# Optimization experiments

Measured on AMD Instinct MI355X. Metric: run time of the kernel, lower is better.

The kernel has to match this reference:

```python
import jax, jax.numpy as jnp
import numpy as np

HIDDEN = 2048
NHEADS = 16
NKV = 4
HEAD_DIM = 128
B, T = 2, 2048


def setup_inputs() -> dict:
    key = jax.random.key(0)
    ks = jax.random.split(key, 7)
    x = jax.random.normal(ks[0], (B, T, HIDDEN), dtype=jnp.float32)
    # rope tables [T, head_dim//2]
    inv_freq = 1.0 / (10000.0 ** (jnp.arange(0, HEAD_DIM // 2, dtype=jnp.float32) / (HEAD_DIM // 2)))
    pos = jnp.arange(T, dtype=jnp.float32)
    ang = pos[:, None] * inv_freq[None, :]
    cos, sin = jnp.cos(ang), jnp.sin(ang)
    s = 0.02
    wq = jax.random.normal(ks[1], (HIDDEN, NHEADS * HEAD_DIM), dtype=jnp.float32) * s
    wk = jax.random.normal(ks[2], (HIDDEN, NKV * HEAD_DIM), dtype=jnp.float32) * s
    wv = jax.random.normal(ks[3], (HIDDEN, NKV * HEAD_DIM), dtype=jnp.float32) * s
    wo = jax.random.normal(ks[4], (NHEADS * HEAD_DIM, HIDDEN), dtype=jnp.float32) * s
    return {"x": x, "cos": cos, "sin": sin, "wq": wq, "wk": wk, "wv": wv, "wo": wo}


def _apply_rope(x, cos, sin):
    # x: [B, H, T, D]; cos/sin: [T, D//2]
    hd = x.shape[-1]
    x1, x2 = x[..., : hd // 2], x[..., hd // 2 :]
    c = cos[None, None, : x.shape[2], :]
    s = sin[None, None, : x.shape[2], :]
    return jnp.concatenate([x1 * c - x2 * s, x2 * c + x1 * s], axis=-1)


def reference(x, cos, sin, wq, wk, wv, wo):
    Bb, Tt, _ = x.shape
    q = (x @ wq).reshape(Bb, Tt, NHEADS, HEAD_DIM).transpose(0, 2, 1, 3)  # [B,H,T,D]
    k = (x @ wk).reshape(Bb, Tt, NKV, HEAD_DIM).transpose(0, 2, 1, 3)    # [B,Hk,T,D]
    v = (x @ wv).reshape(Bb, Tt, NKV, HEAD_DIM).transpose(0, 2, 1, 3)
    q = _apply_rope(q, cos, sin)
    k = _apply_rope(k, cos, sin)
    groups = NHEADS // NKV
    k = jnp.repeat(k, groups, axis=1)  # [B,H,T,D]
    v = jnp.repeat(v, groups, axis=1)
    scale = 1.0 / jnp.sqrt(jnp.asarray(HEAD_DIM, dtype=x.dtype))
    scores = jnp.einsum("bhqd,bhkd->bhqk", q, k) * scale
    causal = jnp.tril(jnp.ones((Tt, Tt), dtype=bool))
    scores = jnp.where(causal[None, None, :, :], scores, jnp.asarray(-jnp.inf, dtype=scores.dtype))
    attn = jax.nn.softmax(scores, axis=-1)
    out = jnp.einsum("bhqk,bhkd->bhqd", attn, v)
    out = out.transpose(0, 2, 1, 3).reshape(Bb, Tt, NHEADS * HEAD_DIM)
    return out @ wo
```

## Files before the change

kernel.cpp:

```cpp
#include <hip/hip_runtime.h>

#define HIDDEN 2048
#define NHEADS 16
#define NKV 4
#define HEAD_DIM 128
#define BB 2
#define TT 2048
#define MROWS (BB * TT)
#define NQKV (NHEADS * HEAD_DIM + 2 * NKV * HEAD_DIM)

typedef __attribute__((ext_vector_type(8))) short short8;
typedef __attribute__((ext_vector_type(4))) float f32x4;

#if __has_builtin(__builtin_amdgcn_exp2f)
#define EXP2F __builtin_amdgcn_exp2f
#else
#define EXP2F exp2f
#endif

__device__ __forceinline__ unsigned short f2bf(float f) {
    unsigned int u = __float_as_uint(f);
    unsigned int r = u + 0x7fffu + ((u >> 16) & 1u);
    return (unsigned short)(r >> 16);
}
__device__ __forceinline__ float b2f(unsigned short h) {
    return __uint_as_float(((unsigned int)h) << 16);
}

__device__ __forceinline__ void load_lds_16(const void* g, void* l) {
    __builtin_amdgcn_global_load_lds((const __attribute__((address_space(1))) unsigned int*)g,
                                     (__attribute__((address_space(3))) unsigned int*)l,
                                     16, 0, 0);
}

__global__ void cast_x_kernel(const float* __restrict__ x, unsigned short* __restrict__ xb) {
    int i = blockIdx.x * 256 + threadIdx.x;
    float4 v = ((const float4*)x)[i];
    ushort4 o;
    o.x = f2bf(v.x); o.y = f2bf(v.y); o.z = f2bf(v.z); o.w = f2bf(v.w);
    ((ushort4*)xb)[i] = o;
}

__global__ void pack_wqkvT_kernel(const float* __restrict__ wq, const float* __restrict__ wk,
                                  const float* __restrict__ wv, unsigned short* __restrict__ out) {
    __shared__ float tile[32][33];
    int n0 = blockIdx.x * 32, k0 = blockIdx.y * 32;
    int tx = threadIdx.x, ty = threadIdx.y;
#pragma unroll
    for (int i = 0; i < 32; i += 8) {
        int k = k0 + ty + i;
        int n = n0 + tx;
        float v;
        if (n < 2048)      v = wq[(size_t)k * 2048 + n];
        else if (n < 2560) v = wk[(size_t)k * 512 + (n - 2048)];
        else               v = wv[(size_t)k * 512 + (n - 2560)];
        tile[ty + i][tx] = v;
    }
    __syncthreads();
#pragma unroll
    for (int i = 0; i < 32; i += 8) {
        int n = n0 + ty + i;
        int k = k0 + tx;
        out[(size_t)n * HIDDEN + k] = f2bf(tile[tx][ty + i]);
    }
}

__global__ void pack_woT_kernel(const float* __restrict__ wo, unsigned short* __restrict__ out) {
    __shared__ float tile[32][33];
    int n0 = blockIdx.x * 32, k0 = blockIdx.y * 32;
    int tx = threadIdx.x, ty = threadIdx.y;
#pragma unroll
    for (int i = 0; i < 32; i += 8)
        tile[ty + i][tx] = wo[(size_t)(k0 + ty + i) * HIDDEN + n0 + tx];
    __syncthreads();
#pragma unroll
    for (int i = 0; i < 32; i += 8)
        out[(size_t)(n0 + ty + i) * HIDDEN + k0 + tx] = f2bf(tile[tx][ty + i]);
}

__global__ __launch_bounds__(512, 2) void gemm192_kernel(const unsigned short* __restrict__ A,
                                                         const unsigned short* __restrict__ Bt,
                                                         unsigned short* __restrict__ C) {
    const int N = NQKV, K = HIDDEN, NBX = 16;
    __shared__ __align__(16) unsigned short sA[2][256 * 64];
    __shared__ __align__(16) unsigned short sB[2][192 * 64];
    const int tid = threadIdx.x;
    const int lane = tid & 63, w = tid >> 6;
    const int quad = lane >> 4, l15 = lane & 15;
    const int wrM = w >> 2, wcN = w & 3;

    const int nwg = gridDim.x;
    const int bswz = (blockIdx.x & 7) * (nwg >> 3) + (blockIdx.x >> 3);
    const int m0 = (bswz / NBX) * 256;
    const int n0 = (bswz % NBX) * 192;

    const int lr = tid >> 3;
    const int sc = (tid & 7) ^ (lr & 7);
    const unsigned short* gA = A + (size_t)(m0 + lr) * K + sc * 8;
    const unsigned short* gB = Bt + (size_t)(n0 + lr) * K + sc * 8;
    const size_t jstep = (size_t)64 * K;

    const int s0 = (quad ^ (l15 & 7)) * 8;
    const int s1 = ((4 | quad) ^ (l15 & 7)) * 8;

    f32x4 acc[8][3];
    const f32x4 z4 = {0.f, 0.f, 0.f, 0.f};
#pragma unroll
    for (int mi = 0; mi < 8; ++mi)
#pragma unroll
        for (int ni = 0; ni < 3; ++ni) acc[mi][ni] = z4;

#pragma unroll
    for (int j = 0; j < 4; ++j)
        load_lds_16(gA + (size_t)j * jstep, &sA[0][j * 4096 + w * 512]);
#pragma unroll
    for (int j = 0; j < 3; ++j)
        load_lds_16(gB + (size_t)j * jstep, &sB[0][j * 4096 + w * 512]);

    const int NT = K >> 6;
    for (int kt = 0; kt < NT; ++kt) {
        const int buf = kt & 1;
        const unsigned short* bA = &sA[buf][0];
        const unsigned short* bB = &sB[buf][0];

        __builtin_amdgcn_s_barrier();
        if (kt + 1 < NT) {
            const size_t kof = (size_t)(kt + 1) * 64;
#pragma unroll
            for (int j = 0; j < 4; ++j)
                load_lds_16(gA + (size_t)j * jstep + kof, &sA[buf ^ 1][j * 4096 + w * 512]);
#pragma unroll
            for (int j = 0; j < 3; ++j)
                load_lds_16(gB + (size_t)j * jstep + kof, &sB[buf ^ 1][j * 4096 + w * 512]);
            __asm__ volatile("s_waitcnt vmcnt(7)" ::: "memory");
        } else {
            __asm__ volatile("s_waitcnt vmcnt(0)" ::: "memory");
        }
        __builtin_amdgcn_s_barrier();

        short8 bf0[3], bf1[3];
#pragma unroll
        for (int ni = 0; ni < 3; ++ni) {
            const unsigned short* br = bB + (wcN * 48 + ni * 16 + l15) * 64;
            bf0[ni] = *(const short8*)(br + s0);
            bf1[ni] = *(const short8*)(br + s1);
        }
#pragma unroll
        for (int ph = 0; ph < 4; ++ph) {
            short8 af0[2], af1[2];
#pragma unroll
            for (int mm = 0; mm < 2; ++mm) {
                const unsigned short* ar = bA + (wrM * 128 + (ph * 2 + mm) * 16 + l15) * 64;
                af0[mm] = *(const short8*)(ar + s0);
                af1[mm] = *(const short8*)(ar + s1);
            }
#pragma unroll
            for (int mm = 0; mm < 2; ++mm)
#pragma unroll
                for (int ni = 0; ni < 3; ++ni) {
                    acc[ph * 2 + mm][ni] =
                        __builtin_amdgcn_mfma_f32_16x16x32_bf16(af0[mm], bf0[ni], acc[ph * 2 + mm][ni], 0, 0, 0);
                    acc[ph * 2 + mm][ni] =
                        __builtin_amdgcn_mfma_f32_16x16x32_bf16(af1[mm], bf1[ni], acc[ph * 2 + mm][ni], 0, 0, 0);
                }
        }
    }

#pragma unroll
    for (int mi = 0; mi < 8; ++mi)
#pragma unroll
        for (int ni = 0; ni < 3; ++ni)
#pragma unroll
            for (int r = 0; r < 4; ++r) {
                int gr = m0 + wrM * 128 + mi * 16 + quad * 4 + r;
                int gc = n0 + wcN * 48 + ni * 16 + l15;
                C[(size_t)gr * N + gc] = f2bf(acc[mi][ni][r]);
            }
}

__global__ __launch_bounds__(512, 2) void gemm256n128_kernel(const unsigned short* __restrict__ A,
                                                             const unsigned short* __restrict__ Bt,
                                                             float* __restrict__ C,
                                                             int M, int N, int K, int NBX) {
    __shared__ __align__(16) unsigned short sA[2][256 * 64];
    __shared__ __align__(16) unsigned short sB[2][128 * 64];
    const int tid = threadIdx.x;
    const int lane = tid & 63, w = tid >> 6;
    const int quad = lane >> 4, l15 = lane & 15;
    const int wrM = w >> 1, wcN = w & 1;

    const int nwg = gridDim.x;
    const int bswz = (blockIdx.x & 7) * (nwg >> 3) + (blockIdx.x >> 3);
    const int m0 = (bswz / NBX) * 256;
    const int n0 = (bswz % NBX) * 128;

    const int lr = tid >> 3;
    const int sc = (tid & 7) ^ (lr & 7);
    const unsigned short* gA = A + (size_t)(m0 + lr) * K + sc * 8;
    const unsigned short* gB = Bt + (size_t)(n0 + lr) * K + sc * 8;
    const size_t jstep = (size_t)64 * K;

    const int s0 = (quad ^ (l15 & 7)) * 8;
    const int s1 = ((4 | quad) ^ (l15 & 7)) * 8;

    f32x4 acc[4][4];
    const f32x4 z4 = {0.f, 0.f, 0.f, 0.f};
#pragma unroll
    for (int mi = 0; mi < 4; ++mi)
#pragma unroll
        for (int ni = 0; ni < 4; ++ni) acc[mi][ni] = z4;

#pragma unroll
    for (int j = 0; j < 4; ++j)
        load_lds_16(gA + (size_t)j * jstep, &sA[0][j * 4096 + w * 512]);
#pragma unroll
    for (int j = 0; j < 2; ++j)
        load_lds_16(gB + (size_t)j * jstep, &sB[0][j * 4096 + w * 512]);

    const int NT = K >> 6;
    for (int kt = 0; kt < NT; ++kt) {
        const int buf = kt & 1;
        const unsigned short* bA = &sA[buf][0];
        const unsigned short* bB = &sB[buf][0];

        __builtin_amdgcn_s_barrier();
        if (kt + 1 < NT) {
            const size_t kof = (size_t)(kt + 1) * 64;
#pragma unroll
            for (int j = 0; j < 4; ++j)
                load_lds_16(gA + (size_t)j * jstep + kof, &sA[buf ^ 1][j * 4096 + w * 512]);
#pragma unroll
            for (int j = 0; j < 2; ++j)
                load_lds_16(gB + (size_t)j * jstep + kof, &sB[buf ^ 1][j * 4096 + w * 512]);
            __asm__ volatile("s_waitcnt vmcnt(6)" ::: "memory");
        } else {
            __asm__ volatile("s_waitcnt vmcnt(0)" ::: "memory");
        }
        __builtin_amdgcn_s_barrier();

        short8 bf0[4], bf1[4];
#pragma unroll
        for (int ni = 0; ni < 4; ++ni) {
            const unsigned short* br = bB + (wcN * 64 + ni * 16 + l15) * 64;
            bf0[ni] = *(const short8*)(br + s0);
            bf1[ni] = *(const short8*)(br + s1);
        }
#pragma unroll
        for (int ph = 0; ph < 4; ++ph) {
            short8 af0, af1;
            {
                const unsigned short* ar = bA + (wrM * 64 + ph * 16 + l15) * 64;
                af0 = *(const short8*)(ar + s0);
                af1 = *(const short8*)(ar + s1);
            }
#pragma unroll
            for (int ni = 0; ni < 4; ++ni) {
                acc[ph][ni] = __builtin_amdgcn_mfma_f32_16x16x32_bf16(af0, bf0[ni], acc[ph][ni], 0, 0, 0);
                acc[ph][ni] = __builtin_amdgcn_mfma_f32_16x16x32_bf16(af1, bf1[ni], acc[ph][ni], 0, 0, 0);
            }
        }
    }

#pragma unroll
    for (int mi = 0; mi < 4; ++mi)
#pragma unroll
        for (int ni = 0; ni < 4; ++ni)
#pragma unroll
            for (int r = 0; r < 4; ++r) {
                int gr = m0 + wrM * 64 + mi * 16 + quad * 4 + r;
                int gc = n0 + wcN * 64 + ni * 16 + l15;
                C[(size_t)gr * N + gc] = acc[mi][ni][r];
            }
}

#define QP (MROWS * NHEADS * 64)
#define KP (MROWS * NKV * 64)
#define QSCL (0.08838834764831845f * 1.4426950408889634f)
__global__ void rope_kernel(const unsigned short* __restrict__ qkv,
                            const float* __restrict__ cosb, const float* __restrict__ sinb,
                            unsigned short* __restrict__ Q, unsigned short* __restrict__ K) {
    int tid = blockIdx.x * 256 + threadIdx.x;
    if (tid < QP) {
        int d = tid & 63;
        int h = (tid >> 6) & 15;
        int row = tid >> 10;
        int t = row & (TT - 1), b = row >> 11;
        float x1 = b2f(qkv[(size_t)row * NQKV + h * 128 + d]);
        float x2 = b2f(qkv[(size_t)row * NQKV + h * 128 + d + 64]);
        float c = cosb[t * 64 + d], s = sinb[t * 64 + d];
        unsigned short* dst = Q + ((size_t)(b * NHEADS + h) * TT + t) * 128 + d;
        dst[0]  = f2bf((x1 * c - x2 * s) * QSCL);
        dst[64] = f2bf((x2 * c + x1 * s) * QSCL);
    } else {
        int p = tid - QP;
        int d = p & 63;
        int kh = (p >> 6) & 3;
        int row = p >> 8;
        int t = row & (TT - 1), b = row >> 11;
        float x1 = b2f(qkv[(size_t)row * NQKV + 2048 + kh * 128 + d]);
        float x2 = b2f(qkv[(size_t)row * NQKV + 2048 + kh * 128 + d + 64]);
        float c = cosb[t * 64 + d], s = sinb[t * 64 + d];
        unsigned short* dst = K + ((size_t)(b * NKV + kh) * TT + t) * 128 + d;
        dst[0]  = f2bf(x1 * c - x2 * s);
        dst[64] = f2bf(x2 * c + x1 * s);
    }
}

__global__ void vtrans_kernel(const unsigned short* __restrict__ qkv,
                              unsigned short* __restrict__ Vt) {
    __shared__ unsigned short tile[32][33];
    int t0 = blockIdx.x * 32, d0 = blockIdx.y * 32, bz = blockIdx.z;
    int b = bz >> 2, kh = bz & 3;
    int tx = threadIdx.x, ty = threadIdx.y;
#pragma unroll
    for (int i = 0; i < 32; i += 8)
        tile[ty + i][tx] = qkv[(size_t)(b * TT + t0 + ty + i) * NQKV + 2560 + kh * 128 + d0 + tx];
    __syncthreads();
#pragma unroll
    for (int i = 0; i < 32; i += 8)
        Vt[((size_t)bz * 128 + d0 + ty + i) * TT + t0 + tx] = tile[tx][ty + i];
}

__global__ __launch_bounds__(256, 3) void flash_kernel(const unsigned short* __restrict__ Qb,
                                                       const unsigned short* __restrict__ Kb,
                                                       const unsigned short* __restrict__ Vtb,
                                                       unsigned short* __restrict__ Ob,
                                                       unsigned short* __restrict__ Po,
                                                       float* __restrict__ Pl) {
    __shared__ __align__(16) unsigned short sK[2][64 * 128];
    __shared__ __align__(16) unsigned short sV[128 * 64];

    const int tid = threadIdx.x;
    const int w = tid >> 6, lane = tid & 63;
    const int quad = lane >> 4, l15 = lane & 15;
    const int r7 = l15 & 7;

    const int lin = blockIdx.x;
    const int member = lin >> 8;
    const int rem = lin & 255;
    const int h = rem & 15;
    const int b = (rem >> 4) & 1;
    const int j = rem >> 5;
    int qb, kvlo, kvhi;
    bool partial;
    if (member == 2) {
        qb = j; kvlo = 0; kvhi = (qb + 1) * 128; partial = false;
    } else {
        qb = 15 - j;
        int half = (qb + 1) * 64;
        kvlo = member ? half : 0;
        kvhi = member ? (qb + 1) * 128 : half;
        partial = true;
    }
    const int q0 = qb * 128;
    const int ntile = (kvhi - kvlo) >> 6;
    const int kvh = h >> 2;
    const unsigned short* Qh = Qb + (size_t)(b * NHEADS + h) * TT * 128;
    const unsigned short* Kh = Kb + (size_t)(b * NKV + kvh) * TT * 128;
    const unsigned short* Vth = Vtb + (size_t)(b * NKV + kvh) * 128 * TT;

    const int wrow0 = q0 + w * 32;

    const int kr = lane >> 4;
    const unsigned short* gKe = Kh + (size_t)(w * 16 + kr) * 128 + (((lane & 15) ^ kr) * 8);
    const unsigned short* gKo = Kh + (size_t)(w * 16 + 4 + kr) * 128 + (((lane & 15) ^ (4 + kr)) * 8);
    const int vr = lane >> 3;
    const unsigned short* gV0 = Vth + (size_t)(w * 32 + vr) * TT + (((lane & 7) ^ vr) * 8);

    short8 aq[2][4];
#pragma unroll
    for (int mi = 0; mi < 2; ++mi)
#pragma unroll
        for (int dk = 0; dk < 4; ++dk)
            aq[mi][dk] = *(const short8*)(Qh + (size_t)(wrow0 + mi * 16 + l15) * 128 + dk * 32 + quad * 8);

    f32x4 accO[2][8];
    float accLc[2] = {0.f, 0.f};
    const f32x4 z4 = {0.f, 0.f, 0.f, 0.f};
#pragma unroll
    for (int mi = 0; mi < 2; ++mi)
#pragma unroll
        for (int nb = 0; nb < 8; ++nb) accO[mi][nb] = z4;

#pragma unroll
    for (int g = 0; g < 4; ++g) {
        const unsigned short* src = (g & 1) ? gKo : gKe;
        load_lds_16(src + (size_t)(kvlo + (g >> 1) * 8) * 128, &sK[0][(w * 4 + g) * 512]);
    }

    for (int it = 0; it < ntile; ++it) {
        const int cur = it & 1;
        const int kv0 = kvlo + it * 64;
        __asm__ volatile("s_waitcnt vmcnt(0)" ::: "memory");
        __builtin_amdgcn_s_barrier();
#pragma unroll
        for (int g = 0; g < 4; ++g)
            load_lds_16(gV0 + (size_t)(g * 8) * TT + kv0, &sV[(w * 4 + g) * 512]);
        const bool hasn = (it + 1 < ntile);
        if (hasn) {
#pragma unroll
            for (int g = 0; g < 4; ++g) {
                const unsigned short* src = (g & 1) ? gKo : gKe;
                load_lds_16(src + (size_t)(kv0 + 64 + (g >> 1) * 8) * 128, &sK[cur ^ 1][(w * 4 + g) * 512]);
            }
        }
        const bool compute = (kv0 <= wrow0 + 31);
        short8 ap[2][2];
        if (compute) {
            f32x4 st[4][2];
#pragma unroll
            for (int t = 0; t < 4; ++t)
#pragma unroll
                for (int h2 = 0; h2 < 2; ++h2) st[t][h2] = z4;
            __builtin_amdgcn_s_setprio(1);
#pragma unroll
            for (int t = 0; t < 4; ++t) {
#pragma unroll
                for (int dk = 0; dk < 4; ++dk) {
                    short8 ak = *(const short8*)(&sK[cur][(t * 16 + l15) * 128 + ((dk * 4 + quad) ^ r7) * 8]);
                    st[t][0] = __builtin_amdgcn_mfma_f32_16x16x32_bf16(ak, aq[0][dk], st[t][0], 0, 0, 0);
                    st[t][1] = __builtin_amdgcn_mfma_f32_16x16x32_bf16(ak, aq[1][dk], st[t][1], 0, 0, 0);
                }
            }
            __builtin_amdgcn_s_setprio(0);
            unsigned int pk32[4][2][2];
#pragma unroll
            for (int h2 = 0; h2 < 2; ++h2) {
                const int qg = wrow0 + h2 * 16 + l15;
#pragma unroll
                for (int t = 0; t < 4; ++t) {
                    const int kvb = kv0 + t * 16 + quad * 4;
                    const bool nm = (kv0 + t * 16 + 15) > (wrow0 + h2 * 16);
                    float pv[4];
#pragma unroll
                    for (int r = 0; r < 4; ++r) {
                        float p = EXP2F(st[t][h2][r]);
                        if (nm) p = (kvb + r <= qg) ? p : 0.f;
                        pv[r] = p;
                    }
                    accLc[h2] += (pv[0] + pv[1]) + (pv[2] + pv[3]);
                    __asm__("v_cvt_pk_bf16_f32 %0, %1, %2" : "=v"(pk32[t][h2][0]) : "v"(pv[0]), "v"(pv[1]));
                    __asm__("v_cvt_pk_bf16_f32 %0, %1, %2" : "=v"(pk32[t][h2][1]) : "v"(pv[2]), "v"(pv[3]));
                }
            }
#pragma unroll
            for (int h2 = 0; h2 < 2; ++h2)
#pragma unroll
                for (int kf = 0; kf < 2; ++kf) {
                    union { unsigned int u[4]; short8 s8; } W;
#pragma unroll
                    for (int wdx = 0; wdx < 4; ++wdx) {
                        int srcl = (2 * (quad & 1) + (wdx >> 1)) * 16 + l15;
                        unsigned int a0 = (unsigned int)__shfl((int)pk32[2 * kf][h2][wdx & 1], srcl, 64);
                        unsigned int a1 = (unsigned int)__shfl((int)pk32[2 * kf + 1][h2][wdx & 1], srcl, 64);
                        W.u[wdx] = (quad >> 1) ? a1 : a0;
                    }
                    ap[h2][kf] = W.s8;
                }
        }
        if (hasn) { __asm__ volatile("s_waitcnt vmcnt(4)" ::: "memory"); }
        else      { __asm__ volatile("s_waitcnt vmcnt(0)" ::: "memory"); }
        __builtin_amdgcn_s_barrier();
        if (compute) {
            __builtin_amdgcn_s_setprio(1);
#pragma unroll
            for (int nb = 0; nb < 8; ++nb) {
                short8 bv0 = *(const short8*)(&sV[(nb * 16 + l15) * 64 + ((quad) ^ r7) * 8]);
                short8 bv1 = *(const short8*)(&sV[(nb * 16 + l15) * 64 + ((4 + quad) ^ r7) * 8]);
#pragma unroll
                for (int mi = 0; mi < 2; ++mi) {
                    accO[mi][nb] = __builtin_amdgcn_mfma_f32_16x16x32_bf16(ap[mi][0], bv0, accO[mi][nb], 0, 0, 0);
                    accO[mi][nb] = __builtin_amdgcn_mfma_f32_16x16x32_bf16(ap[mi][1], bv1, accO[mi][nb], 0, 0, 0);
                }
            }
            __builtin_amdgcn_s_setprio(0);
        }
    }

    float Lr[2][4];
#pragma unroll
    for (int mi = 0; mi < 2; ++mi) {
        float v = accLc[mi];
        v += __shfl_xor(v, 16, 64);
        v += __shfl_xor(v, 32, 64);
#pragma unroll
        for (int r = 0; r < 4; ++r)
            Lr[mi][r] = __shfl(v, quad * 4 + r, 64);
    }

    __syncthreads();
    unsigned short* sPw = &sV[0] + w * 2048;

    if (!partial) {
        float inv[2][4];
#pragma unroll
        for (int mi = 0; mi < 2; ++mi)
#pragma unroll
            for (int r = 0; r < 4; ++r) inv[mi][r] = 1.0f / Lr[mi][r];
        const size_t obase = ((size_t)b * TT + wrow0) * (NHEADS * HEAD_DIM) + h * 128;
#pragma unroll
        for (int half = 0; half < 2; ++half) {
            __asm__ volatile("s_waitcnt lgkmcnt(0)" ::: "memory");
#pragma unroll
            for (int mi = 0; mi < 2; ++mi)
#pragma unroll
                for (int nb2 = 0; nb2 < 4; ++nb2)
#pragma unroll
                    for (int r = 0; r < 4; ++r) {
                        const int row = mi * 16 + quad * 4 + r;
                        sPw[row * 64 + (((2 * nb2 + (l15 >> 3)) ^ (row & 7)) * 8) + r7] =
                            f2bf(accO[mi][half * 4 + nb2][r] * inv[mi][r]);
                    }
            __asm__ volatile("s_waitcnt lgkmcnt(0)" ::: "memory");
#pragma unroll
            for (int pass = 0; pass < 4; ++pass) {
                int row2 = pass * 8 + (lane >> 3);
                short8 vv = *(const short8*)(&sPw[row2 * 64 + (((lane & 7) ^ (row2 & 7)) * 8)]);
                *(short8*)(Ob + obase + (size_t)row2 * (NHEADS * HEAD_DIM) + half * 64 + (lane & 7) * 8) = vv;
            }
        }
    } else {
        const size_t pbase = ((size_t)(member * 2 + b) * 1024 + (wrow0 - 1024)) * 2048 + h * 128;
#pragma unroll
        for (int half = 0; half < 2; ++half) {
            __asm__ volatile("s_waitcnt lgkmcnt(0)" ::: "memory");
#pragma unroll
            for (int mi = 0; mi < 2; ++mi)
#pragma unroll
                for (int nb2 = 0; nb2 < 4; ++nb2)
#pragma unroll
                    for (int r = 0; r < 4; ++r) {
                        const int row = mi * 16 + quad * 4 + r;
                        sPw[row * 64 + (((2 * nb2 + (l15 >> 3)) ^ (row & 7)) * 8) + r7] =
                            f2bf(accO[mi][half * 4 + nb2][r]);
                    }
            __asm__ volatile("s_waitcnt lgkmcnt(0)" ::: "memory");
#pragma unroll
            for (int pass = 0; pass < 4; ++pass) {
                int row2 = pass * 8 + (lane >> 3);
                short8 vv = *(const short8*)(&sPw[row2 * 64 + (((lane & 7) ^ (row2 & 7)) * 8)]);
                *(short8*)(Po + pbase + (size_t)row2 * 2048 + half * 64 + (lane & 7) * 8) = vv;
            }
        }
        float* plb = Pl + ((size_t)(member * 2 + b) * 16 + h) * 1024 + (wrow0 - 1024);
        if (l15 == 0) {
#pragma unroll
            for (int mi = 0; mi < 2; ++mi)
#pragma unroll
                for (int r = 0; r < 4; ++r)
                    plb[mi * 16 + quad * 4 + r] = Lr[mi][r];
        }
    }
}

__global__ void merge_kernel(const unsigned short* __restrict__ Po, const float* __restrict__ Pl,
                             unsigned short* __restrict__ attn) {
    int gid = blockIdx.x * 256 + threadIdx.x;
    size_t e8 = (size_t)gid * 8;
    int col = (int)(e8 & 2047);
    int rl  = (int)((e8 >> 11) & 1023);
    int b   = (int)(e8 >> 21);
    int h   = col >> 7;
    size_t i0 = ((size_t)b * 1024 + rl) * 2048 + col;
    size_t i1 = ((size_t)(2 + b) * 1024 + rl) * 2048 + col;
    float l = Pl[((size_t)b * 16 + h) * 1024 + rl] + Pl[((size_t)(2 + b) * 16 + h) * 1024 + rl];
    float inv = 1.0f / l;
    union { uint4 v; unsigned short u[8]; } a, c, o;
    a.v = *(const uint4*)(Po + i0);
    c.v = *(const uint4*)(Po + i1);
#pragma unroll
    for (int k = 0; k < 8; ++k)
        o.u[k] = f2bf((b2f(a.u[k]) + b2f(c.u[k])) * inv);
    *(uint4*)(attn + ((size_t)b * 2048 + 1024 + rl) * 2048 + col) = o.v;
}

extern "C" void kernel_launch(void* const* d_in, const int* in_sizes, int n_in,
                              void* d_out, int out_size, void* d_ws, size_t ws_size,
                              hipStream_t stream) {
    const float* x    = (const float*)d_in[0];
    const float* cosb = (const float*)d_in[1];
    const float* sinb = (const float*)d_in[2];
    const float* wq   = (const float*)d_in[3];
    const float* wk   = (const float*)d_in[4];
    const float* wv   = (const float*)d_in[5];
    const float* wo   = (const float*)d_in[6];
    float* out = (float*)d_out;

    char* ws = (char*)d_ws;
    unsigned short* xb    = (unsigned short*)(ws);
    unsigned short* wqkvT = (unsigned short*)(ws + (16u << 20));
    unsigned short* woT   = (unsigned short*)(ws + (28u << 20));
    unsigned short* qkv   = (unsigned short*)(ws + (36u << 20));
    unsigned short* Qbuf  = (unsigned short*)(ws + (60u << 20));
    unsigned short* Kbuf  = (unsigned short*)(ws + (76u << 20));
    unsigned short* Vt    = (unsigned short*)(ws + (80u << 20));
    unsigned short* attn  = (unsigned short*)(ws + (84u << 20));
    unsigned short* Po    = (unsigned short*)(ws);
    float*          Pl    = (float*)(ws + (16u << 20));

    cast_x_kernel<<<(MROWS * HIDDEN) / 4 / 256, 256, 0, stream>>>(x, xb);
    pack_wqkvT_kernel<<<dim3(NQKV / 32, HIDDEN / 32), dim3(32, 8), 0, stream>>>(wq, wk, wv, wqkvT);
    pack_woT_kernel<<<dim3(HIDDEN / 32, HIDDEN / 32), dim3(32, 8), 0, stream>>>(wo, woT);

    gemm192_kernel<<<dim3(256), 512, 0, stream>>>(xb, wqkvT, qkv);

    rope_kernel<<<(QP + KP) / 256, 256, 0, stream>>>(qkv, cosb, sinb, Qbuf, Kbuf);
    vtrans_kernel<<<dim3(TT / 32, HEAD_DIM / 32, BB * NKV), dim3(32, 8), 0, stream>>>(qkv, Vt);

    flash_kernel<<<dim3(768), 256, 0, stream>>>(Qbuf, Kbuf, Vt, attn, Po, Pl);
    merge_kernel<<<dim3(2048), 256, 0, stream>>>(Po, Pl, attn);

    gemm256n128_kernel<<<dim3((MROWS / 256) * (HIDDEN / 128)), 512, 0, stream>>>(
        attn, woT, out, MROWS, HIDDEN, HIDDEN, HIDDEN / 128);
}
```

Before: 307.4 us.

## Interleave next-tile global loads with MFMA phases in QKV GEMM main loop

Restructures the QKV projection GEMM K-loop into four explicit phases. Each phase reads A fragments from LDS, issues a slice of the next tile's global-to-LDS loads, then runs its MFMAs at raised wave priority, with barriers and partial vmcnt waits between phases. The goal is to spread memory traffic across the compute instead of issuing every prefetch at the top of the iteration behind a double barrier. The cost is more barriers per iteration and hand-tuned waitcnt values that must stay consistent with the load ordering.

```diff
diff --git a/kernel.cpp b/kernel.cpp
--- a/kernel.cpp
+++ b/kernel.cpp
@@ -110,33 +110,23 @@
 #pragma unroll
         for (int ni = 0; ni < 3; ++ni) acc[mi][ni] = z4;
 
-#pragma unroll
-    for (int j = 0; j < 4; ++j)
-        load_lds_16(gA + (size_t)j * jstep, &sA[0][j * 4096 + w * 512]);
-#pragma unroll
-    for (int j = 0; j < 3; ++j)
-        load_lds_16(gB + (size_t)j * jstep, &sB[0][j * 4096 + w * 512]);
+    load_lds_16(gB + (size_t)0 * jstep, &sB[0][0 * 4096 + w * 512]);
+    load_lds_16(gB + (size_t)1 * jstep, &sB[0][1 * 4096 + w * 512]);
+    load_lds_16(gB + (size_t)2 * jstep, &sB[0][2 * 4096 + w * 512]);
+    load_lds_16(gA + (size_t)0 * jstep, &sA[0][0 * 4096 + w * 512]);
+    load_lds_16(gA + (size_t)2 * jstep, &sA[0][2 * 4096 + w * 512]);
+    load_lds_16(gA + (size_t)1 * jstep, &sA[0][1 * 4096 + w * 512]);
+    load_lds_16(gA + (size_t)3 * jstep, &sA[0][3 * 4096 + w * 512]);
+    __asm__ volatile("s_waitcnt vmcnt(2)" ::: "memory");
+    __builtin_amdgcn_s_barrier();
 
     const int NT = K >> 6;
     for (int kt = 0; kt < NT; ++kt) {
-        const int buf = kt & 1;
+        const int buf = kt & 1, nxt = buf ^ 1;
         const unsigned short* bA = &sA[buf][0];
         const unsigned short* bB = &sB[buf][0];
-
-        __builtin_amdgcn_s_barrier();
-        if (kt + 1 < NT) {
-            const size_t kof = (size_t)(kt + 1) * 64;
-#pragma unroll
-            for (int j = 0; j < 4; ++j)
-                load_lds_16(gA + (size_t)j * jstep + kof, &sA[buf ^ 1][j * 4096 + w * 512]);
-#pragma unroll
-            for (int j = 0; j < 3; ++j)
-                load_lds_16(gB + (size_t)j * jstep + kof, &sB[buf ^ 1][j * 4096 + w * 512]);
-            __asm__ volatile("s_waitcnt vmcnt(7)" ::: "memory");
-        } else {
-            __asm__ volatile("s_waitcnt vmcnt(0)" ::: "memory");
-        }
-        __builtin_amdgcn_s_barrier();
+        const bool hasn = (kt + 1 < NT);
+        const size_t kof = (size_t)(kt + 1) * 64;
 
         short8 bf0[3], bf1[3];
 #pragma unroll
@@ -145,25 +135,104 @@
             bf0[ni] = *(const short8*)(br + s0);
             bf1[ni] = *(const short8*)(br + s1);
         }
-#pragma unroll
-        for (int ph = 0; ph < 4; ++ph) {
-            short8 af0[2], af1[2];
-#pragma unroll
-            for (int mm = 0; mm < 2; ++mm) {
-                const unsigned short* ar = bA + (wrM * 128 + (ph * 2 + mm) * 16 + l15) * 64;
-                af0[mm] = *(const short8*)(ar + s0);
-                af1[mm] = *(const short8*)(ar + s1);
-            }
-#pragma unroll
-            for (int mm = 0; mm < 2; ++mm)
-#pragma unroll
-                for (int ni = 0; ni < 3; ++ni) {
-                    acc[ph * 2 + mm][ni] =
-                        __builtin_amdgcn_mfma_f32_16x16x32_bf16(af0[mm], bf0[ni], acc[ph * 2 + mm][ni], 0, 0, 0);
-                    acc[ph * 2 + mm][ni] =
-                        __builtin_amdgcn_mfma_f32_16x16x32_bf16(af1[mm], bf1[ni], acc[ph * 2 + mm][ni], 0, 0, 0);
-                }
-        }
+        short8 a00[2], a01[2];
+#pragma unroll
+        for (int mm = 0; mm < 2; ++mm) {
+            const unsigned short* ar = bA + (wrM * 128 + mm * 16 + l15) * 64;
+            a00[mm] = *(const short8*)(ar + s0);
+            a01[mm] = *(const short8*)(ar + s1);
+        }
+        if (hasn) {
+            load_lds_16(gB + (size_t)0 * jstep + kof, &sB[nxt][0 * 4096 + w * 512]);
+            load_lds_16(gB + (size_t)1 * jstep + kof, &sB[nxt][1 * 4096 + w * 512]);
+        }
+        __builtin_amdgcn_s_barrier();
+        __asm__ volatile("s_waitcnt lgkmcnt(0)" ::: "memory");
+        __builtin_amdgcn_s_setprio(1);
+#pragma unroll
+        for (int mm = 0; mm < 2; ++mm)
+#pragma unroll
+            for (int ni = 0; ni < 3; ++ni) {
+                acc[mm][ni] = __builtin_amdgcn_mfma_f32_16x16x32_bf16(a00[mm], bf0[ni], acc[mm][ni], 0, 0, 0);
+                acc[mm][ni] = __builtin_amdgcn_mfma_f32_16x16x32_bf16(a01[mm], bf1[ni], acc[mm][ni], 0, 0, 0);
+            }
+        __builtin_amdgcn_s_setprio(0);
+        __builtin_amdgcn_s_barrier();
+
+        short8 a10[2], a11[2];
+#pragma unroll
+        for (int mm = 0; mm < 2; ++mm) {
+            const unsigned short* ar = bA + (wrM * 128 + (2 + mm) * 16 + l15) * 64;
+            a10[mm] = *(const short8*)(ar + s0);
+            a11[mm] = *(const short8*)(ar + s1);
+        }
+        if (hasn) {
+            load_lds_16(gB + (size_t)2 * jstep + kof, &sB[nxt][2 * 4096 + w * 512]);
+            load_lds_16(gA + (size_t)0 * jstep + kof, &sA[nxt][0 * 4096 + w * 512]);
+            __asm__ volatile("s_waitcnt vmcnt(4)" ::: "memory");
+        } else {
+            __asm__ volatile("s_waitcnt vmcnt(0)" ::: "memory");
+        }
+        __builtin_amdgcn_s_barrier();
+        __asm__ volatile("s_waitcnt lgkmcnt(0)" ::: "memory");
+        __builtin_amdgcn_s_setprio(1);
+#pragma unroll
+        for (int mm = 0; mm < 2; ++mm)
+#pragma unroll
+            for (int ni = 0; ni < 3; ++ni) {
+                acc[2 + mm][ni] = __builtin_amdgcn_mfma_f32_16x16x32_bf16(a10[mm], bf0[ni], acc[2 + mm][ni], 0, 0, 0);
+                acc[2 + mm][ni] = __builtin_amdgcn_mfma_f32_16x16x32_bf16(a11[mm], bf1[ni], acc[2 + mm][ni], 0, 0, 0);
+            }
+        __builtin_amdgcn_s_setprio(0);
+        __builtin_amdgcn_s_barrier();
+
+        short8 a20[2], a21[2];
+#pragma unroll
+        for (int mm = 0; mm < 2; ++mm) {
+            const unsigned short* ar = bA + (wrM * 128 + (4 + mm) * 16 + l15) * 64;
+            a20[mm] = *(const short8*)(ar + s0);
+            a21[mm] = *(const short8*)(ar + s1);
+        }
+        if (hasn) {
+            load_lds_16(gA + (size_t)2 * jstep + kof, &sA[nxt][2 * 4096 + w * 512]);
+            load_lds_16(gA + (size_t)1 * jstep + kof, &sA[nxt][1 * 4096 + w * 512]);
+        }
+        __builtin_amdgcn_s_barrier();
+        __asm__ volatile("s_waitcnt lgkmcnt(0)" ::: "memory");
+        __builtin_amdgcn_s_setprio(1);
+#pragma unroll
+        for (int mm = 0; mm < 2; ++mm)
+#pragma unroll
+            for (int ni = 0; ni < 3; ++ni) {
+                acc[4 + mm][ni] = __builtin_amdgcn_mfma_f32_16x16x32_bf16(a20[mm], bf0[ni], acc[4 + mm][ni], 0, 0, 0);
+                acc[4 + mm][ni] = __builtin_amdgcn_mfma_f32_16x16x32_bf16(a21[mm], bf1[ni], acc[4 + mm][ni], 0, 0, 0);
+            }
+        __builtin_amdgcn_s_setprio(0);
+        __builtin_amdgcn_s_barrier();
+
+        short8 a30[2], a31[2];
+#pragma unroll
+        for (int mm = 0; mm < 2; ++mm) {
+            const unsigned short* ar = bA + (wrM * 128 + (6 + mm) * 16 + l15) * 64;
+            a30[mm] = *(const short8*)(ar + s0);
+            a31[mm] = *(const short8*)(ar + s1);
+        }
+        if (hasn) {
+            load_lds_16(gA + (size_t)3 * jstep + kof, &sA[nxt][3 * 4096 + w * 512]);
+            __asm__ volatile("s_waitcnt vmcnt(2)" ::: "memory");
+        }
+        __builtin_amdgcn_s_barrier();
+        __asm__ volatile("s_waitcnt lgkmcnt(0)" ::: "memory");
+        __builtin_amdgcn_s_setprio(1);
+#pragma unroll
+        for (int mm = 0; mm < 2; ++mm)
+#pragma unroll
+            for (int ni = 0; ni < 3; ++ni) {
+                acc[6 + mm][ni] = __builtin_amdgcn_mfma_f32_16x16x32_bf16(a30[mm], bf0[ni], acc[6 + mm][ni], 0, 0, 0);
+                acc[6 + mm][ni] = __builtin_amdgcn_mfma_f32_16x16x32_bf16(a31[mm], bf1[ni], acc[6 + mm][ni], 0, 0, 0);
+            }
+        __builtin_amdgcn_s_setprio(0);
+        __builtin_amdgcn_s_barrier();
     }
 
 #pragma unroll
```

After: 304.3 us. About the same (-1.0%).
